# Optimization experiments

Measured on AMD Instinct MI355X. Metric: run time of the kernel, lower is better.

Reference implementation:

```python
import jax, jax.numpy as jnp
import numpy as np

B, S, HID = 8, 4096, 4096
NH, HD, ROT = 32, 128, 64  # heads, head_dim, rotary_dim (rotary_percentage=0.5)
FFN = 16384
EPS = 1e-5
SCALE = HD ** -0.5


def _ln1p(x, w, b):
    # LayerNorm1P: layer_norm with (weight + 1)
    mu = jnp.mean(x, axis=-1, keepdims=True)
    var = jnp.var(x, axis=-1, keepdims=True)
    return (x - mu) * jax.lax.rsqrt(var + EPS) * (w + 1.0) + b


def _rope(x, pos):
    # x: [B, NH, ROT] (rotary slice), pos: [B] int. GPT-NeoX style (rotate halves).
    half = ROT // 2
    inv_freq = 1.0 / (10000.0 ** (jnp.arange(0, ROT, 2, dtype=jnp.float32) / ROT))
    ang = pos[:, None].astype(jnp.float32) * inv_freq       # [B, half]
    cos = jnp.cos(ang)[:, None, :].astype(x.dtype)           # [B, 1, half]
    sin = jnp.sin(ang)[:, None, :].astype(x.dtype)
    x1, x2 = x[..., :half], x[..., half:]
    return jnp.concatenate([x1 * cos - x2 * sin, x2 * cos + x1 * sin], axis=-1)


def setup_inputs() -> dict:
    key = jax.random.key(0)
    ks = jax.random.split(key, 12)
    w = lambda k, shp: (jax.random.normal(k, shp, jnp.float32) * 0.02)
    return {
        "hidden_states": jax.random.normal(ks[0], (B, HID), jnp.float32),
        "k_cache": jax.random.normal(ks[1], (B, S, NH, HD), jnp.float32),
        "v_cache": jax.random.normal(ks[2], (B, S, NH, HD), jnp.float32),
        "w_qkv": w(ks[3], (HID, 3 * HID)),
        "w_dense": w(ks[4], (HID, HID)),
        "w_fc1": w(ks[5], (HID, 2 * FFN)),
        "w_fc2": w(ks[6], (FFN, HID)),
        "ln1_w": jax.random.normal(ks[7], (HID,), jnp.float32) * 0.02,
        "ln1_b": jnp.zeros((HID,), jnp.float32),
        "ln2_w": jax.random.normal(ks[8], (HID,), jnp.float32) * 0.02,
        "ln2_b": jnp.zeros((HID,), jnp.float32),
        "positions": jax.random.randint(ks[9], (B,), 0, S, jnp.int64),
    }


def reference(hidden_states, k_cache, v_cache, w_qkv, w_dense, w_fc1, w_fc2,
              ln1_w, ln1_b, ln2_w, ln2_b, positions):
    residual = hidden_states
    x = _ln1p(hidden_states, ln1_w, ln1_b)

    # fused QKV projection, chunk along last dim
    qkv = x @ w_qkv                                          # [B, 3*HID]
    q, k, v = jnp.split(qkv, 3, axis=-1)
    q = q.reshape(B, NH, HD)
    k = k.reshape(B, NH, HD)
    v = v.reshape(B, NH, HD)

    # inline RoPE on first ROT dims of q and new k
    q = jnp.concatenate([_rope(q[..., :ROT], positions), q[..., ROT:]], axis=-1)
    k = jnp.concatenate([_rope(k[..., :ROT], positions), k[..., ROT:]], axis=-1)

    # write new token's k/v into the paged KV cache at its slot
    bidx = jnp.arange(B)
    k_cache = k_cache.at[bidx, positions].set(k)
    v_cache = v_cache.at[bidx, positions].set(v)

    # single-query paged attention over cached keys, causal to current position
    scores = jnp.einsum('bhd,bshd->bhs', q, k_cache) * SCALE  # [B, NH, S]
    valid = jnp.arange(S)[None, None, :] <= positions[:, None, None]
    scores = jnp.where(valid, scores, jnp.finfo(scores.dtype).min)
    probs = jax.nn.softmax(scores, axis=-1)
    attn = jnp.einsum('bhs,bshd->bhd', probs, v_cache).reshape(B, HID)

    hidden_states = residual + attn @ w_dense

    residual = hidden_states
    x = _ln1p(hidden_states, ln2_w, ln2_b)
    h = x @ w_fc1                                            # [B, 2*FFN]
    h1, h2 = jnp.split(h, 2, axis=-1)
    x = (jax.nn.silu(h1) * h2) @ w_fc2                       # SwiGLU
    return residual + x
```

## Files before the change

kernel.cpp:

```cpp
#include <hip/hip_runtime.h>
#include <cstddef>
#include <cstdint>

#define NB 8
#define SEQ 4096
#define HIDDIM 4096
#define NHEAD 32
#define HDIM 128
#define FFNDIM 16384
#define ATTN_SCALE 0.08838834764831845f

__device__ __forceinline__ float wave_sum(float v) {
#pragma unroll
  for (int off = 32; off > 0; off >>= 1) v += __shfl_xor(v, off, 64);
  return v;
}

__device__ __forceinline__ int get_pos(const int* __restrict__ p, int b) {
  const bool is64 = ((p[1] | p[3] | p[5] | p[7]) == 0);
  return is64 ? p[2 * b] : p[b];
}

__global__ __launch_bounds__(256) void ln_rows(const float* __restrict__ in,
                                               const float* __restrict__ w,
                                               const float* __restrict__ bias,
                                               float* __restrict__ out_t) {
  __shared__ float row[HIDDIM];
  __shared__ float red[4];
  const int b = blockIdx.x, t = threadIdx.x;
  float s = 0.f;
  for (int i = t; i < HIDDIM; i += 256) {
    const float v = in[(size_t)b * HIDDIM + i];
    row[i] = v;
    s += v;
  }
  s = wave_sum(s);
  if ((t & 63) == 0) red[t >> 6] = s;
  __syncthreads();
  const float mean = (red[0] + red[1] + red[2] + red[3]) * (1.0f / HIDDIM);
  __syncthreads();
  float vs = 0.f;
  for (int i = t; i < HIDDIM; i += 256) {
    const float d = row[i] - mean;
    vs += d * d;
  }
  vs = wave_sum(vs);
  if ((t & 63) == 0) red[t >> 6] = vs;
  __syncthreads();
  const float var = (red[0] + red[1] + red[2] + red[3]) * (1.0f / HIDDIM);
  const float rs = rsqrtf(var + 1e-5f);
  for (int i = t; i < HIDDIM; i += 256) {
    out_t[(size_t)i * NB + b] = (row[i] - mean) * rs * (w[i] + 1.0f) + bias[i];
  }
}

template <int KCHUNK>
__global__ __launch_bounds__(256, 2) void gemm8(const float* __restrict__ W,
                                                const float* __restrict__ xt,
                                                float* __restrict__ part, int N) {
  const int j0 = (blockIdx.x * 256 + threadIdx.x) * 4;
  const size_t i0 = (size_t)blockIdx.y * KCHUNK;
  const float* __restrict__ wp = W + i0 * N + j0;
  const float* __restrict__ xp = xt + i0 * NB;
  float4 a0 = {0, 0, 0, 0}, a1 = {0, 0, 0, 0}, a2 = {0, 0, 0, 0}, a3 = {0, 0, 0, 0};
  float4 a4 = {0, 0, 0, 0}, a5 = {0, 0, 0, 0}, a6 = {0, 0, 0, 0}, a7 = {0, 0, 0, 0};
#pragma unroll 8
  for (int i = 0; i < KCHUNK; ++i) {
    const float4 w = *reinterpret_cast<const float4*>(wp + (size_t)i * N);
    const float4 xa = *reinterpret_cast<const float4*>(xp + i * NB);
    const float4 xb = *reinterpret_cast<const float4*>(xp + i * NB + 4);
#define ACC4(A, sxx)                                                          \
  A.x = fmaf(sxx, w.x, A.x);                                                  \
  A.y = fmaf(sxx, w.y, A.y);                                                  \
  A.z = fmaf(sxx, w.z, A.z);                                                  \
  A.w = fmaf(sxx, w.w, A.w);
    ACC4(a0, xa.x) ACC4(a1, xa.y) ACC4(a2, xa.z) ACC4(a3, xa.w)
    ACC4(a4, xb.x) ACC4(a5, xb.y) ACC4(a6, xb.z) ACC4(a7, xb.w)
#undef ACC4
  }
  float* op = part + (size_t)blockIdx.y * NB * N + j0;
  *reinterpret_cast<float4*>(op) = a0; op += N;
  *reinterpret_cast<float4*>(op) = a1; op += N;
  *reinterpret_cast<float4*>(op) = a2; op += N;
  *reinterpret_cast<float4*>(op) = a3; op += N;
  *reinterpret_cast<float4*>(op) = a4; op += N;
  *reinterpret_cast<float4*>(op) = a5; op += N;
  *reinterpret_cast<float4*>(op) = a6; op += N;
  *reinterpret_cast<float4*>(op) = a7;
}

__global__ __launch_bounds__(128) void rope_reduce(const float* __restrict__ part, int nchunk,
                                                   const int* __restrict__ posp,
                                                   float* __restrict__ qo,
                                                   float* __restrict__ ko,
                                                   float* __restrict__ vo) {
  const int blk = blockIdx.x;
  const int b = blk >> 5, h = blk & 31;
  const int t = threadIdx.x;
  const int role = t >> 5;
  const int d4 = (t & 31) * 4;
  const int col = h * HDIM + d4;
  __shared__ float qsh[HDIM], ksh[HDIM];
  float4 acc = {0.f, 0.f, 0.f, 0.f};
  if (role < 3) {
    const size_t off = (size_t)role * HIDDIM + col;
    for (int c = 0; c < nchunk; ++c) {
      const float4 p = *reinterpret_cast<const float4*>(
          part + ((size_t)c * NB + b) * (3 * HIDDIM) + off);
      acc.x += p.x; acc.y += p.y; acc.z += p.z; acc.w += p.w;
    }
    if (role == 0) *reinterpret_cast<float4*>(&qsh[d4]) = acc;
    if (role == 1) *reinterpret_cast<float4*>(&ksh[d4]) = acc;
  }
  __syncthreads();
  if (role < 2) {
    const float* sh = role ? ksh : qsh;
    const float pos = (float)get_pos(posp, b);
    float4 o;
    float* ov = &o.x;
#pragma unroll
    for (int j = 0; j < 4; ++j) {
      const int d = d4 + j;
      if (d < 64) {
        const int f = d & 31;
        const float ang = pos * powf(10000.0f, -(float)f * (1.0f / 32.0f));
        const float cs = cosf(ang), sn = sinf(ang);
        ov[j] = (d < 32) ? sh[d] * cs - sh[d + 32] * sn
                         : sh[d] * cs + sh[d - 32] * sn;
      } else {
        ov[j] = sh[d];
      }
    }
    float* dst = (role ? ko : qo) + (size_t)b * HIDDIM + col;
    *reinterpret_cast<float4*>(dst) = o;
  } else if (role == 2) {
    *reinterpret_cast<float4*>(vo + (size_t)b * HIDDIM + col) = acc;
  }
}

__global__ __launch_bounds__(256) void attn_split(
    const float* __restrict__ kc, const float* __restrict__ vc,
    const float* __restrict__ q, const float* __restrict__ kn,
    const float* __restrict__ vn, const int* __restrict__ posp,
    float* __restrict__ Mp, float* __restrict__ Lp, float* __restrict__ Ap) {
  const int c = blockIdx.x, h = blockIdx.y, b = blockIdx.z;
  const int pos = get_pos(posp, b);
  const int s0 = c * 256;
  if (s0 > pos) return;
  const int s1 = min(s0 + 256, pos + 1);
  const int wid = threadIdx.x >> 6, lane = threadIdx.x & 63;
  const int dd = 2 * lane;
  const float2 qv = *reinterpret_cast<const float2*>(q + (size_t)b * HIDDIM + h * HDIM + dd);
  const float* kb = kc + ((size_t)b * SEQ * NHEAD + h) * HDIM + dd;
  const float* vb = vc + ((size_t)b * SEQ * NHEAD + h) * HDIM + dd;
  const float* knp = kn + (size_t)b * HIDDIM + h * HDIM + dd;
  const float* vnp = vn + (size_t)b * HIDDIM + h * HDIM + dd;
  float m = -INFINITY, l = 0.f;
  float2 acc = {0.f, 0.f};
  for (int s = s0 + wid; s < s1; s += 4) {
    const float* kp = (s == pos) ? knp : kb + (size_t)s * (NHEAD * HDIM);
    const float* vp = (s == pos) ? vnp : vb + (size_t)s * (NHEAD * HDIM);
    const float2 kk = *reinterpret_cast<const float2*>(kp);
    const float2 vv = *reinterpret_cast<const float2*>(vp);
    float p = qv.x * kk.x + qv.y * kk.y;
    p = wave_sum(p) * ATTN_SCALE;
    const float mn = fmaxf(m, p);
    const float cf = __expf(m - mn);
    const float pw = __expf(p - mn);
    l = l * cf + pw;
    acc.x = acc.x * cf + pw * vv.x;
    acc.y = acc.y * cf + pw * vv.y;
    m = mn;
  }
  __shared__ float sm[4], sl[4], sa[4][HDIM];
  sa[wid][dd] = acc.x;
  sa[wid][dd + 1] = acc.y;
  if (lane == 0) { sm[wid] = m; sl[wid] = l; }
  __syncthreads();
  if (threadIdx.x < HDIM) {
    const int d = threadIdx.x;
    const float M = fmaxf(fmaxf(sm[0], sm[1]), fmaxf(sm[2], sm[3]));
    float L = 0.f, A = 0.f;
#pragma unroll
    for (int w2 = 0; w2 < 4; ++w2) {
      const float e = __expf(sm[w2] - M);
      L += e * sl[w2];
      A += e * sa[w2][d];
    }
    const size_t idx = (size_t)(b * NHEAD + h) * 16 + c;
    if (d == 0) { Mp[idx] = M; Lp[idx] = L; }
    Ap[idx * HDIM + d] = A;
  }
}

__global__ __launch_bounds__(128) void attn_combine(
    const float* __restrict__ Mp, const float* __restrict__ Lp,
    const float* __restrict__ Ap, const int* __restrict__ posp,
    float* __restrict__ out_t) {
  const int blk = blockIdx.x;
  const int b = blk >> 5, h = blk & 31;
  const int d = threadIdx.x;
  const int nc = get_pos(posp, b) / 256 + 1;
  const size_t base = (size_t)(b * NHEAD + h) * 16;
  float M = -INFINITY;
  for (int c = 0; c < nc; ++c) M = fmaxf(M, Mp[base + c]);
  float L = 0.f, A = 0.f;
  for (int c = 0; c < nc; ++c) {
    const float e = __expf(Mp[base + c] - M);
    L += e * Lp[base + c];
    A += e * Ap[(base + c) * HDIM + d];
  }
  out_t[(size_t)(h * HDIM + d) * NB + b] = A / L;
}

__global__ __launch_bounds__(128) void reduce_add(const float* __restrict__ part, int nchunk,
                                                  const float* __restrict__ base,
                                                  float* __restrict__ out) {
  const int i4 = blockIdx.x * 128 + threadIdx.x;
  const float4* b4 = reinterpret_cast<const float4*>(base);
  const float4* p4 = reinterpret_cast<const float4*>(part);
  float4 v = b4[i4];
  for (int c = 0; c < nchunk; ++c) {
    const float4 p = p4[(size_t)c * (NB * HIDDIM / 4) + i4];
    v.x += p.x; v.y += p.y; v.z += p.z; v.w += p.w;
  }
  reinterpret_cast<float4*>(out)[i4] = v;
}

__global__ __launch_bounds__(256) void gate_silu(const float* __restrict__ part, int nchunk,
                                                 float* __restrict__ gt) {
  const int j4 = (blockIdx.x * 256 + threadIdx.x) * 4;
  const int b = blockIdx.y;
  float4 h1 = {0.f, 0.f, 0.f, 0.f}, h2 = {0.f, 0.f, 0.f, 0.f};
  for (int c = 0; c < nchunk; ++c) {
    const float* p = part + ((size_t)c * NB + b) * (2 * FFNDIM);
    const float4 a = *reinterpret_cast<const float4*>(p + j4);
    const float4 g = *reinterpret_cast<const float4*>(p + FFNDIM + j4);
    h1.x += a.x; h1.y += a.y; h1.z += a.z; h1.w += a.w;
    h2.x += g.x; h2.y += g.y; h2.z += g.z; h2.w += g.w;
  }
  const float* h1v = &h1.x;
  const float* h2v = &h2.x;
#pragma unroll
  for (int j = 0; j < 4; ++j) {
    const float g = (h1v[j] / (1.f + __expf(-h1v[j]))) * h2v[j];
    gt[(size_t)(j4 + j) * NB + b] = g;
  }
}

extern "C" void kernel_launch(void* const* d_in, const int* in_sizes, int n_in,
                              void* d_out, int out_size, void* d_ws, size_t ws_size,
                              hipStream_t stream) {
  const float* hs = (const float*)d_in[0];
  const float* kc = (const float*)d_in[1];
  const float* vc = (const float*)d_in[2];
  const float* wqkv = (const float*)d_in[3];
  const float* wdense = (const float*)d_in[4];
  const float* wfc1 = (const float*)d_in[5];
  const float* wfc2 = (const float*)d_in[6];
  const float* ln1w = (const float*)d_in[7];
  const float* ln1b = (const float*)d_in[8];
  const float* ln2w = (const float*)d_in[9];
  const float* ln2b = (const float*)d_in[10];
  const int* posp = (const int*)d_in[11];
  float* out = (float*)d_out;

  float* ws = (float*)d_ws;
  float* x1t = ws;
  float* qws = x1t + 32768;
  float* kws = qws + 32768;
  float* vws = kws + 32768;
  float* attnt = vws + 32768;
  float* hidden2 = attnt + 32768;
  float* x2t = hidden2 + 32768;
  float* gt = x2t + 32768;
  float* Mp = gt + 131072;
  float* Lp = Mp + 4096;
  float* Ap = Lp + 4096;
  float* part = Ap + 524288;

  ln_rows<<<8, 256, 0, stream>>>(hs, ln1w, ln1b, x1t);
  gemm8<64><<<dim3(12, 64), 256, 0, stream>>>(wqkv, x1t, part, 3 * HIDDIM);
  rope_reduce<<<256, 128, 0, stream>>>(part, 64, posp, qws, kws, vws);
  attn_split<<<dim3(16, NHEAD, NB), 256, 0, stream>>>(kc, vc, qws, kws, vws, posp, Mp, Lp, Ap);
  attn_combine<<<256, 128, 0, stream>>>(Mp, Lp, Ap, posp, attnt);
  gemm8<64><<<dim3(4, 64), 256, 0, stream>>>(wdense, attnt, part, HIDDIM);
  reduce_add<<<64, 128, 0, stream>>>(part, 64, hs, hidden2);
  ln_rows<<<8, 256, 0, stream>>>(hidden2, ln2w, ln2b, x2t);
  gemm8<256><<<dim3(32, 16), 256, 0, stream>>>(wfc1, x2t, part, 2 * FFNDIM);
  gate_silu<<<dim3(16, NB), 256, 0, stream>>>(part, 16, gt);
  gemm8<256><<<dim3(4, 64), 256, 0, stream>>>(wfc2, gt, part, HIDDIM);
  reduce_add<<<64, 128, 0, stream>>>(part, 64, hidden2, out);
}
```

Baseline: 434.0 us.

## Widen attention loads to float4 with half-wave tokens and retune GEMM splits

```diff
diff --git a/kernel.cpp b/kernel.cpp
--- a/kernel.cpp
+++ b/kernel.cpp
@@ -55,16 +55,16 @@
 }
 
 template <int KCHUNK>
-__global__ __launch_bounds__(256, 2) void gemm8(const float* __restrict__ W,
-                                                const float* __restrict__ xt,
-                                                float* __restrict__ part, int N) {
+__global__ __launch_bounds__(256) void gemm8(const float* __restrict__ W,
+                                             const float* __restrict__ xt,
+                                             float* __restrict__ part, int N) {
   const int j0 = (blockIdx.x * 256 + threadIdx.x) * 4;
   const size_t i0 = (size_t)blockIdx.y * KCHUNK;
   const float* __restrict__ wp = W + i0 * N + j0;
   const float* __restrict__ xp = xt + i0 * NB;
   float4 a0 = {0, 0, 0, 0}, a1 = {0, 0, 0, 0}, a2 = {0, 0, 0, 0}, a3 = {0, 0, 0, 0};
   float4 a4 = {0, 0, 0, 0}, a5 = {0, 0, 0, 0}, a6 = {0, 0, 0, 0}, a7 = {0, 0, 0, 0};
-#pragma unroll 8
+#pragma unroll 4
   for (int i = 0; i < KCHUNK; ++i) {
     const float4 w = *reinterpret_cast<const float4*>(wp + (size_t)i * N);
     const float4 xa = *reinterpret_cast<const float4*>(xp + i * NB);
@@ -149,40 +149,48 @@
   if (s0 > pos) return;
   const int s1 = min(s0 + 256, pos + 1);
   const int wid = threadIdx.x >> 6, lane = threadIdx.x & 63;
-  const int dd = 2 * lane;
-  const float2 qv = *reinterpret_cast<const float2*>(q + (size_t)b * HIDDIM + h * HDIM + dd);
-  const float* kb = kc + ((size_t)b * SEQ * NHEAD + h) * HDIM + dd;
-  const float* vb = vc + ((size_t)b * SEQ * NHEAD + h) * HDIM + dd;
-  const float* knp = kn + (size_t)b * HIDDIM + h * HDIM + dd;
-  const float* vnp = vn + (size_t)b * HIDDIM + h * HDIM + dd;
-  float m = -INFINITY, l = 0.f;
-  float2 acc = {0.f, 0.f};
-  for (int s = s0 + wid; s < s1; s += 4) {
+  const int half = lane >> 5;
+  const int d4 = (lane & 31) * 4;
+  const float4 qv = *reinterpret_cast<const float4*>(q + (size_t)b * HIDDIM + h * HDIM + d4);
+  const float* kb = kc + ((size_t)b * SEQ * NHEAD + h) * HDIM + d4;
+  const float* vb = vc + ((size_t)b * SEQ * NHEAD + h) * HDIM + d4;
+  const float* knp = kn + (size_t)b * HIDDIM + h * HDIM + d4;
+  const float* vnp = vn + (size_t)b * HIDDIM + h * HDIM + d4;
+  float m = -1e30f, l = 0.f;
+  float4 acc = {0.f, 0.f, 0.f, 0.f};
+  for (int sb = s0; sb < s1; sb += 8) {
+    const int s = sb + wid * 2 + half;
     const float* kp = (s == pos) ? knp : kb + (size_t)s * (NHEAD * HDIM);
     const float* vp = (s == pos) ? vnp : vb + (size_t)s * (NHEAD * HDIM);
-    const float2 kk = *reinterpret_cast<const float2*>(kp);
-    const float2 vv = *reinterpret_cast<const float2*>(vp);
-    float p = qv.x * kk.x + qv.y * kk.y;
-    p = wave_sum(p) * ATTN_SCALE;
+    const float4 kk = *reinterpret_cast<const float4*>(kp);
+    const float4 vv = *reinterpret_cast<const float4*>(vp);
+    float p = qv.x * kk.x + qv.y * kk.y + qv.z * kk.z + qv.w * kk.w;
+#pragma unroll
+    for (int off = 16; off > 0; off >>= 1) p += __shfl_xor(p, off, 64);
+    p = (s < s1) ? p * ATTN_SCALE : -2e30f;
     const float mn = fmaxf(m, p);
     const float cf = __expf(m - mn);
     const float pw = __expf(p - mn);
     l = l * cf + pw;
     acc.x = acc.x * cf + pw * vv.x;
     acc.y = acc.y * cf + pw * vv.y;
+    acc.z = acc.z * cf + pw * vv.z;
+    acc.w = acc.w * cf + pw * vv.w;
     m = mn;
   }
-  __shared__ float sm[4], sl[4], sa[4][HDIM];
-  sa[wid][dd] = acc.x;
-  sa[wid][dd + 1] = acc.y;
-  if (lane == 0) { sm[wid] = m; sl[wid] = l; }
+  __shared__ float sm[8], sl[8], sa[8][HDIM];
+  const int st = wid * 2 + half;
+  *reinterpret_cast<float4*>(&sa[st][d4]) = acc;
+  if ((lane & 31) == 0) { sm[st] = m; sl[st] = l; }
   __syncthreads();
   if (threadIdx.x < HDIM) {
     const int d = threadIdx.x;
-    const float M = fmaxf(fmaxf(sm[0], sm[1]), fmaxf(sm[2], sm[3]));
+    float M = -1e30f;
+#pragma unroll
+    for (int w2 = 0; w2 < 8; ++w2) M = fmaxf(M, sm[w2]);
     float L = 0.f, A = 0.f;
 #pragma unroll
-    for (int w2 = 0; w2 < 4; ++w2) {
+    for (int w2 = 0; w2 < 8; ++w2) {
       const float e = __expf(sm[w2] - M);
       L += e * sl[w2];
       A += e * sa[w2][d];
@@ -202,7 +210,7 @@
   const int d = threadIdx.x;
   const int nc = get_pos(posp, b) / 256 + 1;
   const size_t base = (size_t)(b * NHEAD + h) * 16;
-  float M = -INFINITY;
+  float M = -1e30f;
   for (int c = 0; c < nc; ++c) M = fmaxf(M, Mp[base + c]);
   float L = 0.f, A = 0.f;
   for (int c = 0; c < nc; ++c) {
@@ -280,12 +288,12 @@
   float* part = Ap + 524288;
 
   ln_rows<<<8, 256, 0, stream>>>(hs, ln1w, ln1b, x1t);
-  gemm8<64><<<dim3(12, 64), 256, 0, stream>>>(wqkv, x1t, part, 3 * HIDDIM);
-  rope_reduce<<<256, 128, 0, stream>>>(part, 64, posp, qws, kws, vws);
+  gemm8<128><<<dim3(12, 32), 256, 0, stream>>>(wqkv, x1t, part, 3 * HIDDIM);
+  rope_reduce<<<256, 128, 0, stream>>>(part, 32, posp, qws, kws, vws);
   attn_split<<<dim3(16, NHEAD, NB), 256, 0, stream>>>(kc, vc, qws, kws, vws, posp, Mp, Lp, Ap);
   attn_combine<<<256, 128, 0, stream>>>(Mp, Lp, Ap, posp, attnt);
-  gemm8<64><<<dim3(4, 64), 256, 0, stream>>>(wdense, attnt, part, HIDDIM);
-  reduce_add<<<64, 128, 0, stream>>>(part, 64, hs, hidden2);
+  gemm8<128><<<dim3(4, 32), 256, 0, stream>>>(wdense, attnt, part, HIDDIM);
+  reduce_add<<<64, 128, 0, stream>>>(part, 32, hs, hidden2);
   ln_rows<<<8, 256, 0, stream>>>(hidden2, ln2w, ln2b, x2t);
   gemm8<256><<<dim3(32, 16), 256, 0, stream>>>(wfc1, x2t, part, 2 * FFNDIM);
   gate_silu<<<dim3(16, NB), 256, 0, stream>>>(part, 16, gt);
```

Result: faster. 422.8 us (-2.6%).
